# Kernel optimization log

Measured on AMD Instinct MI355X. Metric: run time of the kernel, lower is better.

Reference implementation:

```python
import jax, jax.numpy as jnp
import numpy as np

QBITS = 8
QMIN, QMAX = -(2 ** (QBITS - 1)), 2 ** (QBITS - 1) - 1  # qint8: -128..127


def fq_act(x):
    """Per-tensor affine fake-quant (observer = min/max of tensor), with STE."""
    mn = jnp.minimum(jnp.min(x), 0.0)
    mx = jnp.maximum(jnp.max(x), 0.0)
    scale = jnp.maximum((mx - mn) / (QMAX - QMIN), 1e-8)
    zp = QMIN - jnp.round(mn / scale)
    q = jnp.clip(jnp.round(x / scale) + zp, QMIN, QMAX)
    y = (q - zp) * scale
    return x + jax.lax.stop_gradient(y - x)


def fq_w(w):
    """Per-tensor symmetric weight fake-quant, with STE."""
    scale = jnp.maximum(jnp.max(jnp.abs(w)) / QMAX, 1e-8)
    y = jnp.clip(jnp.round(w / scale), QMIN, QMAX) * scale
    return w + jax.lax.stop_gradient(y - w)


def setup_inputs() -> dict:
    key = jax.random.key(0)
    ks = jax.random.split(key, 8)
    B, T, F, K = 32, 1024, 512, 31
    return {
        "x": jax.random.normal(ks[0], (B, T, F), jnp.float32),
        "ln_scale": jnp.ones((F,), jnp.float32),
        "ln_bias": jnp.zeros((F,), jnp.float32),
        "w1": jax.random.normal(ks[1], (2 * F, F), jnp.float32) * 0.02,
        "b1": jax.random.normal(ks[2], (2 * F,), jnp.float32) * 0.02,
        "dw_w": jax.random.normal(ks[3], (F, 1, K), jnp.float32) * 0.1,
        "dw_b": jax.random.normal(ks[4], (F,), jnp.float32) * 0.02,
        "bn_gamma": jnp.ones((F,), jnp.float32),
        "bn_beta": jnp.zeros((F,), jnp.float32),
        "bn_mean": jnp.zeros((F,), jnp.float32),
        "bn_var": jax.random.uniform(ks[5], (F,), jnp.float32, 0.5, 1.5),
        "w2": jax.random.normal(ks[6], (F, F), jnp.float32) * 0.02,
        "b2": jax.random.normal(ks[7], (F,), jnp.float32) * 0.02,
    }


def reference(x, ln_scale, ln_bias, w1, b1, dw_w, dw_b,
              bn_gamma, bn_beta, bn_mean, bn_var, w2, b2):
    F = x.shape[-1]
    # --- custom L1 layer norm, fake-quant in/out ---
    t = fq_act(x)
    t = t - jnp.mean(t, axis=-1, keepdims=True)
    t = t / (jnp.sum(jnp.abs(t), axis=-1, keepdims=True) / F + 1e-5)
    t = t * ln_scale + ln_bias
    t = fq_act(t)
    # --- pointwise conv 1 (linear F -> 2F), quant-wrapped ---
    t = fq_act(t)
    t = jnp.einsum("btf,of->bto", t, fq_w(w1)) + b1
    t = fq_act(t)
    # --- GLU, quant-wrapped ---
    t = fq_act(t)
    a, g = jnp.split(t, 2, axis=-1)
    t = a * jax.nn.sigmoid(g)
    t = fq_act(t)
    # --- depthwise conv over time, quant-wrapped ---
    t = jnp.transpose(t, (0, 2, 1))  # [B,F,T]
    t = fq_act(t)
    t = jax.lax.conv_general_dilated(
        t, fq_w(dw_w), window_strides=(1,), padding=[((dw_w.shape[-1] - 1) // 2,) * 2],
        dimension_numbers=("NCH", "OIH", "NCH"), feature_group_count=F,
    ) + dw_b[:, None]
    t = fq_act(t)
    # --- batch norm (eval mode, running stats), quant-wrapped ---
    t = fq_act(t)
    t = (t - bn_mean[:, None]) * (bn_gamma[:, None] / jnp.sqrt(bn_var[:, None] + 1e-5)) + bn_beta[:, None]
    t = fq_act(t)
    t = jnp.transpose(t, (0, 2, 1))  # [B,T,F]
    # --- SiLU activation, quant-wrapped ---
    t = fq_act(t)
    t = jax.nn.silu(t)
    t = fq_act(t)
    # --- pointwise conv 2 (linear F -> F), quant-wrapped ---
    t = fq_act(t)
    t = jnp.einsum("btf,of->bto", t, fq_w(w2)) + b2
    t = fq_act(t)
    return t  # dropout is identity at eval
```

## Files before the change

kernel.cpp:

```cpp
#include <hip/hip_runtime.h>
#include <stdint.h>
#include <math.h>

#define INF __builtin_inff()

typedef __attribute__((ext_vector_type(4))) float f32x4;
typedef __attribute__((ext_vector_type(8))) short s16x8;
typedef __attribute__((ext_vector_type(4))) short s16x4;
typedef __attribute__((ext_vector_type(4))) char c8x4;

#define S_XMN 0
#define S_XMX 1
#define S_T1MN 2
#define S_T1MX 3
#define S_T4MN 4
#define S_T4MX 5
#define S_T7MN 6
#define S_T7MX 7
#define S_CVMN 8
#define S_CVMX 9
#define S_BNMN 10
#define S_BNMX 11
#define S_SIMN 12
#define S_SIMX 13
#define S_T18MN 14
#define S_T18MX 15
#define S_W1 16
#define S_W2 17
#define S_DW 18
#define NSLOT 19

#define NTOT 16777216L

__device__ __forceinline__ unsigned enc(float f) {
  unsigned u = __float_as_uint(f);
  return (u & 0x80000000u) ? ~u : (u | 0x80000000u);
}
__device__ __forceinline__ float dec(unsigned k) {
  return (k & 0x80000000u) ? __uint_as_float(k & 0x7FFFFFFFu) : __uint_as_float(~k);
}

struct FQ { float s, zp; };

__device__ __forceinline__ FQ fq_params(float mn_t, float mx_t) {
  float mn = fminf(mn_t, 0.0f), mx = fmaxf(mx_t, 0.0f);
  FQ p;
  p.s = fmaxf((mx - mn) / 255.0f, 1e-8f);
  p.zp = -128.0f - rintf(mn / p.s);
  return p;
}
__device__ __forceinline__ float fq_apply(float x, FQ p) {
  float q = rintf(x / p.s) + p.zp;
  q = fminf(fmaxf(q, -128.0f), 127.0f);
  return (q - p.zp) * p.s;
}
__device__ __forceinline__ float fq_qmz(float x, FQ p) {
  float q = rintf(x / p.s) + p.zp;
  q = fminf(fmaxf(q, -128.0f), 127.0f);
  return q - p.zp;
}
__device__ __forceinline__ int qidx(float x, FQ p) {
  float q = rintf(x / p.s) + p.zp;
  q = fminf(fmaxf(q, -128.0f), 127.0f);
  return (int)q + 128;
}
__device__ __forceinline__ int qcode(float x, FQ p) {
  float q = rintf(x / p.s) + p.zp;
  q = fminf(fmaxf(q, -128.0f), 127.0f);
  return (int)q;
}
__device__ __forceinline__ void fq_pair(const unsigned* slots, int idx, FQ& p1, FQ& p2) {
  float mn = dec(slots[idx]), mx = dec(slots[idx + 1]);
  p1 = fq_params(mn, mx);
  float ymn = fq_apply(mn, p1), ymx = fq_apply(mx, p1);
  p2 = fq_params(ymn, ymx);
}
__device__ __forceinline__ unsigned short to_bf16(float v) {
  return (unsigned short)(__float_as_uint(v) >> 16);
}

__device__ __forceinline__ void mm_block_atomic(float mn, float mx, unsigned* smn, unsigned* smx) {
#pragma unroll
  for (int o = 32; o > 0; o >>= 1) {
    mn = fminf(mn, __shfl_down(mn, o, 64));
    mx = fmaxf(mx, __shfl_down(mx, o, 64));
  }
  __shared__ float rmn[16], rmx[16];
  int lane = threadIdx.x & 63, wid = threadIdx.x >> 6;
  int nw = blockDim.x >> 6;
  __syncthreads();
  if (lane == 0) { rmn[wid] = mn; rmx[wid] = mx; }
  __syncthreads();
  if (threadIdx.x == 0) {
    for (int i = 1; i < nw; ++i) { mn = fminf(mn, rmn[i]); mx = fmaxf(mx, rmx[i]); }
    atomicMin(smn, enc(mn));
    atomicMax(smx, enc(mx));
  }
}

__device__ __forceinline__ float wave_sum(float v) {
#pragma unroll
  for (int o = 1; o < 64; o <<= 1) v += __shfl_xor(v, o, 64);
  return v;
}

__global__ void k_init(unsigned* __restrict__ slots, const float* __restrict__ gm,
                       const float* __restrict__ vr, float* __restrict__ gs) {
  int i = threadIdx.x;
  if (i < NSLOT) slots[i] = (i < 16) ? ((i & 1) ? enc(-INF) : enc(INF)) : enc(0.0f);
  gs[i] = gm[i] / sqrtf(vr[i] + 1e-5f);
}

__global__ __launch_bounds__(256) void k_redmm(const float* __restrict__ x, unsigned* __restrict__ slots) {
  long i = ((long)blockIdx.x * 256 + threadIdx.x) * 4;
  const long stride = (long)2048 * 256 * 4;
  float mn = INF, mx = -INF;
  for (; i < NTOT; i += stride) {
    f32x4 v = *(const f32x4*)(x + i);
    mn = fminf(mn, fminf(fminf(v.x, v.y), fminf(v.z, v.w)));
    mx = fmaxf(mx, fmaxf(fmaxf(v.x, v.y), fmaxf(v.z, v.w)));
  }
  mm_block_atomic(mn, mx, slots + S_XMN, slots + S_XMX);
}

__global__ __launch_bounds__(256) void k_wabs(const float* __restrict__ w1, const float* __restrict__ w2,
                                              const float* __restrict__ dw, unsigned* __restrict__ slots) {
  int b = blockIdx.x;
  const float* p; int slot; long base;
  if (b < 2048) { p = w1; slot = S_W1; base = (long)b * 256; }
  else if (b < 3072) { p = w2; slot = S_W2; base = (long)(b - 2048) * 256; }
  else { p = dw; slot = S_DW; base = (long)(b - 3072) * 256; }
  float v = fabsf(p[base + threadIdx.x]);
#pragma unroll
  for (int o = 32; o > 0; o >>= 1) v = fmaxf(v, __shfl_down(v, o, 64));
  __shared__ float r[4];
  int lane = threadIdx.x & 63, wid = threadIdx.x >> 6;
  if (lane == 0) r[wid] = v;
  __syncthreads();
  if (threadIdx.x == 0) {
    v = fmaxf(fmaxf(r[0], r[1]), fmaxf(r[2], r[3]));
    atomicMax(slots + slot, enc(v));
  }
}

__global__ __launch_bounds__(256) void k_wq(const float* __restrict__ w1, const float* __restrict__ w2,
    const float* __restrict__ dw, unsigned short* __restrict__ w1q, unsigned short* __restrict__ w2q,
    float* __restrict__ dwq, const unsigned* __restrict__ slots) {
  int b = blockIdx.x;
  if (b < 2048) {
    float s = fmaxf(dec(slots[S_W1]) / 127.0f, 1e-8f);
    long i = (long)b * 256 + threadIdx.x;
    float q = fminf(fmaxf(rintf(w1[i] / s), -128.0f), 127.0f);
    w1q[i] = to_bf16(q);
  } else if (b < 3072) {
    float s = fmaxf(dec(slots[S_W2]) / 127.0f, 1e-8f);
    long i = (long)(b - 2048) * 256 + threadIdx.x;
    float q = fminf(fmaxf(rintf(w2[i] / s), -128.0f), 127.0f);
    w2q[i] = to_bf16(q);
  } else {
    float s = fmaxf(dec(slots[S_DW]) / 127.0f, 1e-8f);
    long i = (long)(b - 3072) * 256 + threadIdx.x;
    float q = fminf(fmaxf(rintf(dw[i] / s), -128.0f), 127.0f);
    dwq[i] = q;
  }
}

__device__ __forceinline__ void ln_core(float* a, const f32x4& sc0, const f32x4& sc1,
                                        const f32x4& bi0, const f32x4& bi1) {
  float s = a[0] + a[1] + a[2] + a[3] + a[4] + a[5] + a[6] + a[7];
  float mean = wave_sum(s) / 512.0f;
#pragma unroll
  for (int j = 0; j < 8; ++j) a[j] -= mean;
  float l1 = fabsf(a[0]) + fabsf(a[1]) + fabsf(a[2]) + fabsf(a[3])
           + fabsf(a[4]) + fabsf(a[5]) + fabsf(a[6]) + fabsf(a[7]);
  float denom = wave_sum(l1) / 512.0f + 1e-5f;
#pragma unroll
  for (int j = 0; j < 4; ++j) {
    a[j]     = fmaf(a[j] / denom,     sc0[j], bi0[j]);
    a[4 + j] = fmaf(a[4 + j] / denom, sc1[j], bi1[j]);
  }
}

__global__ __launch_bounds__(256) void k_lnmm(const float* __restrict__ x, const float* __restrict__ lns,
    const float* __restrict__ lnb, signed char* __restrict__ qx, unsigned* __restrict__ slots) {
  FQ p0 = fq_params(dec(slots[S_XMN]), dec(slots[S_XMX]));
  int lane = threadIdx.x & 63, wv = threadIdx.x >> 6;
  long gw = (long)blockIdx.x * 4 + wv;
  f32x4 sc0 = *(const f32x4*)(lns + lane * 4);
  f32x4 sc1 = *(const f32x4*)(lns + 256 + lane * 4);
  f32x4 bi0 = *(const f32x4*)(lnb + lane * 4);
  f32x4 bi1 = *(const f32x4*)(lnb + 256 + lane * 4);
  float lmn = INF, lmx = -INF;
  for (int r = 0; r < 4; ++r) {
    long row = gw + (long)r * 8192;
    f32x4 v0 = *(const f32x4*)(x + row * 512 + lane * 4);
    f32x4 v1 = *(const f32x4*)(x + row * 512 + 256 + lane * 4);
    float a[8];
    c8x4 c0, c1;
#pragma unroll
    for (int j = 0; j < 4; ++j) {
      int q0 = qcode(v0[j], p0), q1 = qcode(v1[j], p0);
      c0[j] = (signed char)q0; c1[j] = (signed char)q1;
      a[j]     = ((float)q0 - p0.zp) * p0.s;
      a[4 + j] = ((float)q1 - p0.zp) * p0.s;
    }
    *(c8x4*)(qx + row * 512 + lane * 4) = c0;
    *(c8x4*)(qx + row * 512 + 256 + lane * 4) = c1;
    ln_core(a, sc0, sc1, bi0, bi1);
#pragma unroll
    for (int j = 0; j < 8; ++j) { lmn = fminf(lmn, a[j]); lmx = fmaxf(lmx, a[j]); }
  }
  mm_block_atomic(lmn, lmx, slots + S_T1MN, slots + S_T1MX);
}

__global__ __launch_bounds__(256) void k_qa(const signed char* __restrict__ qx, const float* __restrict__ lns,
    const float* __restrict__ lnb, unsigned short* __restrict__ A1, const unsigned* __restrict__ slots) {
  __shared__ unsigned short lut[256];
  FQ p0 = fq_params(dec(slots[S_XMN]), dec(slots[S_XMX]));
  FQ p1, p2; fq_pair(slots, S_T1MN, p1, p2);
  {
    int i = threadIdx.x;
    float y1 = ((float)(i - 128) - p1.zp) * p1.s;
    lut[i] = to_bf16(fq_qmz(y1, p2));
  }
  __syncthreads();
  int lane = threadIdx.x & 63, wv = threadIdx.x >> 6;
  long gw = (long)blockIdx.x * 4 + wv;
  f32x4 sc0 = *(const f32x4*)(lns + lane * 4);
  f32x4 sc1 = *(const f32x4*)(lns + 256 + lane * 4);
  f32x4 bi0 = *(const f32x4*)(lnb + lane * 4);
  f32x4 bi1 = *(const f32x4*)(lnb + 256 + lane * 4);
  for (int r = 0; r < 4; ++r) {
    long row = gw + (long)r * 8192;
    c8x4 c0 = *(const c8x4*)(qx + row * 512 + lane * 4);
    c8x4 c1 = *(const c8x4*)(qx + row * 512 + 256 + lane * 4);
    float a[8];
#pragma unroll
    for (int j = 0; j < 4; ++j) {
      a[j]     = ((float)(int)c0[j] - p0.zp) * p0.s;
      a[4 + j] = ((float)(int)c1[j] - p0.zp) * p0.s;
    }
    ln_core(a, sc0, sc1, bi0, bi1);
    s16x4 q0, q1;
#pragma unroll
    for (int j = 0; j < 4; ++j) {
      q0[j] = (short)lut[qidx(a[j], p1)];
      q1[j] = (short)lut[qidx(a[4 + j], p1)];
    }
    *(s16x4*)(A1 + row * 512 + lane * 4) = q0;
    *(s16x4*)(A1 + row * 512 + 256 + lane * 4) = q1;
  }
}

__global__ __launch_bounds__(256) void k_gemm(const unsigned short* __restrict__ A,
    const unsigned short* __restrict__ Bm, const float* __restrict__ bias,
    float* __restrict__ C, int N, unsigned* __restrict__ slots, int mmIdx, int wIdx, int omIdx) {
  __shared__ __align__(16) unsigned short lA[128 * 64];
  __shared__ __align__(16) unsigned short lB[128 * 64];
  FQ p1, p2; fq_pair(slots, mmIdx, p1, p2);
  float sw = fmaxf(dec(slots[wIdx]) / 127.0f, 1e-8f);
  float sAB = p2.s * sw;
  int tid = threadIdx.x;
  int nbx = gridDim.x;
  int total = nbx * gridDim.y;
  int id = blockIdx.y * nbx + blockIdx.x;
  int chunk = total >> 3;
  int d = (id & 7) * chunk + (id >> 3);
  int m0 = (d / nbx) * 128, n0 = (d % nbx) * 128;
  int lane = tid & 63, wid = tid >> 6;
  int wm = (wid >> 1) * 64, wn = (wid & 1) * 64;
  const f32x4 fz = {0.0f, 0.0f, 0.0f, 0.0f};
  f32x4 acc[4][4];
#pragma unroll
  for (int mi = 0; mi < 4; ++mi)
#pragma unroll
    for (int ni = 0; ni < 4; ++ni) acc[mi][ni] = fz;
  int sr = tid >> 1;
  int scu = (tid & 1) * 32;
  int swz = (sr & 7) * 8;
  const unsigned short* Ag = A + (long)(m0 + sr) * 512 + scu;
  const unsigned short* Bg = Bm + (long)(n0 + sr) * 512 + scu;
  int fr = lane & 15;
  int fc = (lane >> 4) * 8;
  for (int kt = 0; kt < 8; ++kt) {
    s16x8 ra[4], rb[4];
#pragma unroll
    for (int j = 0; j < 4; ++j) {
      ra[j] = *(const s16x8*)(Ag + kt * 64 + j * 8);
      rb[j] = *(const s16x8*)(Bg + kt * 64 + j * 8);
    }
    __syncthreads();
#pragma unroll
    for (int j = 0; j < 4; ++j) {
      *(s16x8*)&lA[sr * 64 + ((scu + j * 8) ^ swz)] = ra[j];
      *(s16x8*)&lB[sr * 64 + ((scu + j * 8) ^ swz)] = rb[j];
    }
    __syncthreads();
#pragma unroll
    for (int ks = 0; ks < 2; ++ks) {
      s16x8 af[4], bfv[4];
#pragma unroll
      for (int mi = 0; mi < 4; ++mi) {
        int r = wm + mi * 16 + fr;
        af[mi] = *(const s16x8*)&lA[r * 64 + ((ks * 32 + fc) ^ ((r & 7) * 8))];
      }
#pragma unroll
      for (int ni = 0; ni < 4; ++ni) {
        int r = wn + ni * 16 + fr;
        bfv[ni] = *(const s16x8*)&lB[r * 64 + ((ks * 32 + fc) ^ ((r & 7) * 8))];
      }
#pragma unroll
      for (int mi = 0; mi < 4; ++mi)
#pragma unroll
        for (int ni = 0; ni < 4; ++ni)
          acc[mi][ni] = __builtin_amdgcn_mfma_f32_16x16x32_bf16(af[mi], bfv[ni], acc[mi][ni], 0, 0, 0);
    }
  }
  float lmn = INF, lmx = -INF;
  int rb0 = m0 + wm + ((lane >> 4) << 2);
  int cb0 = n0 + wn + (lane & 15);
#pragma unroll
  for (int mi = 0; mi < 4; ++mi) {
#pragma unroll
    for (int ni = 0; ni < 4; ++ni) {
      int col = cb0 + ni * 16;
      float bv = bias[col];
#pragma unroll
      for (int r = 0; r < 4; ++r) {
        int rowi = rb0 + mi * 16 + r;
        float v = sAB * acc[mi][ni][r] + bv;
        C[(long)rowi * N + col] = v;
        lmn = fminf(lmn, v); lmx = fmaxf(lmx, v);
      }
    }
  }
  mm_block_atomic(lmn, lmx, slots + omIdx, slots + omIdx + 1);
}

__global__ __launch_bounds__(256) void k_glu(const float* __restrict__ t4, unsigned short* __restrict__ pair,
                                             unsigned* __restrict__ slots) {
  __shared__ float lutf[256];
  __shared__ float sglut[256];
  FQ p1, p2; fq_pair(slots, S_T4MN, p1, p2);
  {
    int i = threadIdx.x;
    float y2 = fq_apply(((float)(i - 128) - p1.zp) * p1.s, p2);
    lutf[i] = y2;
    sglut[i] = 1.0f / (1.0f + expf(-y2));
  }
  __syncthreads();
  long i = ((long)blockIdx.x * 256 + threadIdx.x) * 4;
  const long stride = (long)2048 * 256 * 4;
  float lmn = INF, lmx = -INF;
  for (; i < NTOT; i += stride) {
    long r = i >> 9;
    int c = (int)(i & 511);
    const float* pa = t4 + r * 1024 + c;
    f32x4 av = *(const f32x4*)pa;
    f32x4 gv = *(const f32x4*)(pa + 512);
    s16x4 o;
#pragma unroll
    for (int j = 0; j < 4; ++j) {
      int qa = qidx(av[j], p1);
      int qg = qidx(gv[j], p1);
      o[j] = (short)(unsigned short)(qa | (qg << 8));
      float y = lutf[qa] * sglut[qg];
      lmn = fminf(lmn, y); lmx = fmaxf(lmx, y);
    }
    *(s16x4*)(pair + i) = o;
  }
  mm_block_atomic(lmn, lmx, slots + S_T7MN, slots + S_T7MX);
}

__global__ __launch_bounds__(256) void k_qt7(const unsigned short* __restrict__ pair,
                                             signed char* __restrict__ q7,
                                             const unsigned* __restrict__ slots) {
  __shared__ float lutf[256];
  __shared__ float sglut[256];
  __shared__ signed char lutq[256];
  FQ g1, g2; fq_pair(slots, S_T4MN, g1, g2);
  FQ p1, p2; fq_pair(slots, S_T7MN, p1, p2);
  {
    int i = threadIdx.x;
    float y2 = fq_apply(((float)(i - 128) - g1.zp) * g1.s, g2);
    lutf[i] = y2;
    sglut[i] = 1.0f / (1.0f + expf(-y2));
    float y1 = ((float)(i - 128) - p1.zp) * p1.s;
    float q = fminf(fmaxf(rintf(y1 / p2.s) + p2.zp, -128.0f), 127.0f);
    lutq[i] = (signed char)(int)q;
  }
  __syncthreads();
  long i = ((long)blockIdx.x * 256 + threadIdx.x) * 4;
  const long stride = (long)2048 * 256 * 4;
  for (; i < NTOT; i += stride) {
    s16x4 pv = *(const s16x4*)(pair + i);
    c8x4 o;
#pragma unroll
    for (int j = 0; j < 4; ++j) {
      unsigned u = (unsigned short)pv[j];
      float y = lutf[u & 255] * sglut[u >> 8];
      o[j] = lutq[qidx(y, p1)];
    }
    *(c8x4*)(q7 + i) = o;
  }
}

template<int STORE>
__global__ __launch_bounds__(256) void k_conv(const signed char* __restrict__ q7,
    const float* __restrict__ dwq, const float* __restrict__ dwb,
    signed char* __restrict__ qcv, const float* __restrict__ gs, const float* __restrict__ mu,
    const float* __restrict__ bt, unsigned* __restrict__ slots) {
  __shared__ signed char lutq[256];
  FQ p1, p2; fq_pair(slots, S_T7MN, p1, p2);
  float sdw = fmaxf(dec(slots[S_DW]) / 127.0f, 1e-8f);
  float scv = p2.s * sdw;
  float zp2 = p2.zp;
  FQ c1, c2;
  if (STORE) {
    fq_pair(slots, S_CVMN, c1, c2);
    int i = threadIdx.x;
    float y1 = ((float)(i - 128) - c1.zp) * c1.s;
    float q = fminf(fmaxf(rintf(y1 / c2.s) + c2.zp, -128.0f), 127.0f);
    lutq[i] = (signed char)(int)q;
    __syncthreads();
  }
  int t0 = blockIdx.x * 32;
  int f = blockIdx.y * 256 + threadIdx.x;
  int b = blockIdx.z;
  const signed char* base = q7 + (long)b * 1024 * 512 + f;
  float col[62];
#pragma unroll
  for (int r = 0; r < 62; ++r) {
    int t = t0 - 15 + r;
    float q = 0.0f;
    if ((unsigned)t < 1024u) q = (float)(int)base[(long)t * 512] - zp2;
    col[r] = q;
  }
  float w31[31];
#pragma unroll
  for (int k = 0; k < 31; ++k) w31[k] = dwq[f * 31 + k];
  float bias = dwb[f];
  float gsv = 0.f, muv = 0.f, btv = 0.f;
  if (STORE) { gsv = gs[f]; muv = mu[f]; btv = bt[f]; }
  signed char* orow = STORE ? (qcv + ((long)b * 1024 + t0) * 512 + f) : nullptr;
  float lmn = INF, lmx = -INF;
#pragma unroll
  for (int j = 0; j < 32; ++j) {
    float acc = 0.0f;
#pragma unroll
    for (int k = 0; k < 31; ++k) acc += col[j + k] * w31[k];
    float v = fmaf(scv, acc, bias);
    if (STORE) {
      signed char qc = lutq[qidx(v, c1)];
      orow[(long)j * 512] = qc;
      float y2 = ((float)(int)qc - c2.zp) * c2.s;
      float z = fmaf(y2 - muv, gsv, btv);
      lmn = fminf(lmn, z); lmx = fmaxf(lmx, z);
    } else {
      lmn = fminf(lmn, v); lmx = fmaxf(lmx, v);
    }
  }
  if (STORE) mm_block_atomic(lmn, lmx, slots + S_BNMN, slots + S_BNMX);
  else       mm_block_atomic(lmn, lmx, slots + S_CVMN, slots + S_CVMX);
}

__global__ __launch_bounds__(256) void k_silumm(const signed char* __restrict__ qcv,
    const float* __restrict__ gs, const float* __restrict__ mu, const float* __restrict__ bt,
    unsigned* __restrict__ slots) {
  __shared__ float sillut[256];
  FQ c1, c2; fq_pair(slots, S_CVMN, c1, c2);
  FQ b1q, b2q; fq_pair(slots, S_BNMN, b1q, b2q);
  {
    int i = threadIdx.x;
    float z2 = fq_apply(((float)(i - 128) - b1q.zp) * b1q.s, b2q);
    sillut[i] = z2 * (1.0f / (1.0f + expf(-z2)));
  }
  __syncthreads();
  float s2 = c2.s, zp2 = c2.zp;
  long i = ((long)blockIdx.x * 256 + threadIdx.x) * 4;
  const long stride = (long)2048 * 256 * 4;
  float lmn = INF, lmx = -INF;
  for (; i < NTOT; i += stride) {
    int f0 = (int)(i & 511);
    c8x4 qv = *(const c8x4*)(qcv + i);
    f32x4 g4 = *(const f32x4*)(gs + f0);
    f32x4 m4 = *(const f32x4*)(mu + f0);
    f32x4 b4 = *(const f32x4*)(bt + f0);
#pragma unroll
    for (int j = 0; j < 4; ++j) {
      float y2 = ((float)(int)qv[j] - zp2) * s2;
      float z = fmaf(y2 - m4[j], g4[j], b4[j]);
      float si = sillut[qidx(z, b1q)];
      lmn = fminf(lmn, si); lmx = fmaxf(lmx, si);
    }
  }
  mm_block_atomic(lmn, lmx, slots + S_SIMN, slots + S_SIMX);
}

__global__ __launch_bounds__(256) void k_q2(const signed char* __restrict__ qcv,
    const float* __restrict__ gs, const float* __restrict__ mu, const float* __restrict__ bt,
    unsigned short* __restrict__ A2, const unsigned* __restrict__ slots) {
  __shared__ unsigned short lutc[256];
  FQ c1, c2; fq_pair(slots, S_CVMN, c1, c2);
  FQ b1q, b2q; fq_pair(slots, S_BNMN, b1q, b2q);
  FQ s1q, s2q; fq_pair(slots, S_SIMN, s1q, s2q);
  {
    int i = threadIdx.x;
    float z2 = fq_apply(((float)(i - 128) - b1q.zp) * b1q.s, b2q);
    float si = z2 * (1.0f / (1.0f + expf(-z2)));
    float ys = ((float)(qidx(si, s1q) - 128) - s1q.zp) * s1q.s;
    lutc[i] = to_bf16(fq_qmz(ys, s2q));
  }
  __syncthreads();
  float s2 = c2.s, zp2 = c2.zp;
  long i = ((long)blockIdx.x * 256 + threadIdx.x) * 4;
  const long stride = (long)2048 * 256 * 4;
  for (; i < NTOT; i += stride) {
    int f0 = (int)(i & 511);
    c8x4 qv = *(const c8x4*)(qcv + i);
    f32x4 g4 = *(const f32x4*)(gs + f0);
    f32x4 m4 = *(const f32x4*)(mu + f0);
    f32x4 b4 = *(const f32x4*)(bt + f0);
    s16x4 o;
#pragma unroll
    for (int j = 0; j < 4; ++j) {
      float y2 = ((float)(int)qv[j] - zp2) * s2;
      float z = fmaf(y2 - m4[j], g4[j], b4[j]);
      o[j] = (short)lutc[qidx(z, b1q)];
    }
    *(s16x4*)(A2 + i) = o;
  }
}

__global__ __launch_bounds__(256) void k_final(const float* __restrict__ t18, float* __restrict__ out,
                                               const unsigned* __restrict__ slots) {
  FQ p = fq_params(dec(slots[S_T18MN]), dec(slots[S_T18MX]));
  long i = ((long)blockIdx.x * 256 + threadIdx.x) * 4;
  const long stride = (long)2048 * 256 * 4;
  for (; i < NTOT; i += stride) {
    f32x4 v = *(const f32x4*)(t18 + i);
    f32x4 o;
#pragma unroll
    for (int j = 0; j < 4; ++j) o[j] = fq_apply(v[j], p);
    *(f32x4*)(out + i) = o;
  }
}

extern "C" void kernel_launch(void* const* d_in, const int* in_sizes, int n_in,
                              void* d_out, int out_size, void* d_ws, size_t ws_size,
                              hipStream_t stream) {
  const float* x   = (const float*)d_in[0];
  const float* lns = (const float*)d_in[1];
  const float* lnb = (const float*)d_in[2];
  const float* w1  = (const float*)d_in[3];
  const float* b1  = (const float*)d_in[4];
  const float* dw  = (const float*)d_in[5];
  const float* dwb = (const float*)d_in[6];
  const float* gm  = (const float*)d_in[7];
  const float* bt  = (const float*)d_in[8];
  const float* mu  = (const float*)d_in[9];
  const float* vr  = (const float*)d_in[10];
  const float* w2  = (const float*)d_in[11];
  const float* b2  = (const float*)d_in[12];
  float* out = (float*)d_out;
  char* ws = (char*)d_ws;

  const size_t O_A2  = 16777216;
  const size_t O_T18 = 50331648;
  const size_t O_A1  = 134217728;
  const size_t O_QX  = 167772160;
  const size_t O_WQ  = 184549376;
  const size_t NEED = O_WQ + 1048576 + 524288 + 63488 + 2048 + 256;
  if (ws_size < NEED) return;

  float* t4   = (float*)ws;
  signed char* qcv = (signed char*)ws;
  unsigned short* A2 = (unsigned short*)(ws + O_A2);
  float* t18  = (float*)(ws + O_T18);
  unsigned short* A1 = (unsigned short*)(ws + O_A1);
  unsigned short* pair = (unsigned short*)(ws + O_A1);
  signed char* qx = (signed char*)(ws + O_QX);
  signed char* q7 = (signed char*)(ws + O_QX);
  unsigned short* w1q = (unsigned short*)(ws + O_WQ);
  unsigned short* w2q = (unsigned short*)(ws + O_WQ + 1048576);
  float* dwq = (float*)(ws + O_WQ + 1048576 + 524288);
  float* gs  = (float*)(ws + O_WQ + 1048576 + 524288 + 63488);
  unsigned* slots = (unsigned*)(ws + O_WQ + 1048576 + 524288 + 63488 + 2048);

  k_init<<<1, 512, 0, stream>>>(slots, gm, vr, gs);
  k_wabs<<<3134, 256, 0, stream>>>(w1, w2, dw, slots);
  k_wq<<<3134, 256, 0, stream>>>(w1, w2, dw, w1q, w2q, dwq, slots);
  k_redmm<<<2048, 256, 0, stream>>>(x, slots);
  k_lnmm<<<2048, 256, 0, stream>>>(x, lns, lnb, qx, slots);
  k_qa<<<2048, 256, 0, stream>>>(qx, lns, lnb, A1, slots);
  k_gemm<<<dim3(8, 256), 256, 0, stream>>>(A1, w1q, b1, t4, 1024, slots, S_T1MN, S_W1, S_T4MN);
  k_glu<<<2048, 256, 0, stream>>>(t4, pair, slots);
  k_qt7<<<2048, 256, 0, stream>>>(pair, q7, slots);
  k_conv<0><<<dim3(32, 2, 32), 256, 0, stream>>>(q7, dwq, dwb, nullptr, gs, mu, bt, slots);
  k_conv<1><<<dim3(32, 2, 32), 256, 0, stream>>>(q7, dwq, dwb, qcv, gs, mu, bt, slots);
  k_silumm<<<2048, 256, 0, stream>>>(qcv, gs, mu, bt, slots);
  k_q2<<<2048, 256, 0, stream>>>(qcv, gs, mu, bt, A2, slots);
  k_gemm<<<dim3(4, 256), 256, 0, stream>>>(A2, w2q, b2, t18, 512, slots, S_SIMN, S_W2, S_T18MN);
  k_final<<<2048, 256, 0, stream>>>(t18, out, slots);
}
```

Measured before the change: 731.6 us.

## Use direct global-to-LDS loads in GEMM and transpose depthwise weights

The GEMM tile loads now use global_load_lds to write 16-byte chunks straight into LDS, replacing the register staging pass. The source addresses are XOR-swizzled so the existing read swizzle still matches, and the first-iteration barrier is skipped. Depthwise conv weights are stored transposed as [k][f] so each thread's weight loads coalesce across f. The conv inner product is split into four independent accumulators with launch_bounds(256,1), which shortens the FMA dependency chain at the cost of register pressure and a changed float summation order.

```diff
diff --git a/kernel.cpp b/kernel.cpp
--- a/kernel.cpp
+++ b/kernel.cpp
@@ -79,6 +79,12 @@
   return (unsigned short)(__float_as_uint(v) >> 16);
 }
 
+__device__ __forceinline__ void gload_lds16(const void* g, void* l) {
+  __builtin_amdgcn_global_load_lds(
+      (const __attribute__((address_space(1))) unsigned int*)g,
+      (__attribute__((address_space(3))) unsigned int*)l, 16, 0, 0);
+}
+
 __device__ __forceinline__ void mm_block_atomic(float mn, float mx, unsigned* smn, unsigned* smx) {
 #pragma unroll
   for (int o = 32; o > 0; o >>= 1) {
@@ -145,7 +151,7 @@
 
 __global__ __launch_bounds__(256) void k_wq(const float* __restrict__ w1, const float* __restrict__ w2,
     const float* __restrict__ dw, unsigned short* __restrict__ w1q, unsigned short* __restrict__ w2q,
-    float* __restrict__ dwq, const unsigned* __restrict__ slots) {
+    float* __restrict__ dwqT, const unsigned* __restrict__ slots) {
   int b = blockIdx.x;
   if (b < 2048) {
     float s = fmaxf(dec(slots[S_W1]) / 127.0f, 1e-8f);
@@ -159,9 +165,10 @@
     w2q[i] = to_bf16(q);
   } else {
     float s = fmaxf(dec(slots[S_DW]) / 127.0f, 1e-8f);
-    long i = (long)(b - 3072) * 256 + threadIdx.x;
+    int i = (b - 3072) * 256 + threadIdx.x;
+    int f = i / 31, k = i % 31;
     float q = fminf(fmaxf(rintf(dw[i] / s), -128.0f), 127.0f);
-    dwq[i] = q;
+    dwqT[k * 512 + f] = q;
   }
 }
 
@@ -267,33 +274,35 @@
   int chunk = total >> 3;
   int d = (id & 7) * chunk + (id >> 3);
   int m0 = (d / nbx) * 128, n0 = (d % nbx) * 128;
-  int lane = tid & 63, wid = tid >> 6;
-  int wm = (wid >> 1) * 64, wn = (wid & 1) * 64;
+  int lane = tid & 63, w = tid >> 6;
+  int wm = (w >> 1) * 64, wn = (w & 1) * 64;
   const f32x4 fz = {0.0f, 0.0f, 0.0f, 0.0f};
   f32x4 acc[4][4];
 #pragma unroll
   for (int mi = 0; mi < 4; ++mi)
 #pragma unroll
     for (int ni = 0; ni < 4; ++ni) acc[mi][ni] = fz;
-  int sr = tid >> 1;
-  int scu = (tid & 1) * 32;
-  int swz = (sr & 7) * 8;
-  const unsigned short* Ag = A + (long)(m0 + sr) * 512 + scu;
-  const unsigned short* Bg = Bm + (long)(n0 + sr) * 512 + scu;
+  int r8 = lane >> 3;
+  int c8 = (lane & 7) * 8;
+  int srcc = c8 ^ (r8 * 8);
+  const unsigned short* Abase[4];
+  const unsigned short* Bbase[4];
+#pragma unroll
+  for (int i = 0; i < 4; ++i) {
+    int row = w * 32 + i * 8 + r8;
+    Abase[i] = A + (long)(m0 + row) * 512 + srcc;
+    Bbase[i] = Bm + (long)(n0 + row) * 512 + srcc;
+  }
+  char* lAc = (char*)lA;
+  char* lBc = (char*)lB;
   int fr = lane & 15;
   int fc = (lane >> 4) * 8;
   for (int kt = 0; kt < 8; ++kt) {
-    s16x8 ra[4], rb[4];
-#pragma unroll
-    for (int j = 0; j < 4; ++j) {
-      ra[j] = *(const s16x8*)(Ag + kt * 64 + j * 8);
-      rb[j] = *(const s16x8*)(Bg + kt * 64 + j * 8);
-    }
-    __syncthreads();
-#pragma unroll
-    for (int j = 0; j < 4; ++j) {
-      *(s16x8*)&lA[sr * 64 + ((scu + j * 8) ^ swz)] = ra[j];
-      *(s16x8*)&lB[sr * 64 + ((scu + j * 8) ^ swz)] = rb[j];
+    if (kt) __syncthreads();
+#pragma unroll
+    for (int i = 0; i < 4; ++i) {
+      gload_lds16(Abase[i] + kt * 64, lAc + (w * 4 + i) * 1024);
+      gload_lds16(Bbase[i] + kt * 64, lBc + (w * 4 + i) * 1024);
     }
     __syncthreads();
 #pragma unroll
@@ -406,8 +415,8 @@
 }
 
 template<int STORE>
-__global__ __launch_bounds__(256) void k_conv(const signed char* __restrict__ q7,
-    const float* __restrict__ dwq, const float* __restrict__ dwb,
+__global__ __launch_bounds__(256, 1) void k_conv(const signed char* __restrict__ q7,
+    const float* __restrict__ dwqT, const float* __restrict__ dwb,
     signed char* __restrict__ qcv, const float* __restrict__ gs, const float* __restrict__ mu,
     const float* __restrict__ bt, unsigned* __restrict__ slots) {
   __shared__ signed char lutq[256];
@@ -436,9 +445,9 @@
     if ((unsigned)t < 1024u) q = (float)(int)base[(long)t * 512] - zp2;
     col[r] = q;
   }
-  float w31[31];
-#pragma unroll
-  for (int k = 0; k < 31; ++k) w31[k] = dwq[f * 31 + k];
+  float wv[31];
+#pragma unroll
+  for (int k = 0; k < 31; ++k) wv[k] = dwqT[k * 512 + f];
   float bias = dwb[f];
   float gsv = 0.f, muv = 0.f, btv = 0.f;
   if (STORE) { gsv = gs[f]; muv = mu[f]; btv = bt[f]; }
@@ -446,9 +455,18 @@
   float lmn = INF, lmx = -INF;
 #pragma unroll
   for (int j = 0; j < 32; ++j) {
-    float acc = 0.0f;
-#pragma unroll
-    for (int k = 0; k < 31; ++k) acc += col[j + k] * w31[k];
+    float a0 = 0.f, a1 = 0.f, a2 = 0.f, a3 = 0.f;
+#pragma unroll
+    for (int k = 0; k < 28; k += 4) {
+      a0 += col[j + k]     * wv[k];
+      a1 += col[j + k + 1] * wv[k + 1];
+      a2 += col[j + k + 2] * wv[k + 2];
+      a3 += col[j + k + 3] * wv[k + 3];
+    }
+    a0 += col[j + 28] * wv[28];
+    a1 += col[j + 29] * wv[29];
+    a2 += col[j + 30] * wv[30];
+    float acc = (a0 + a1) + (a2 + a3);
     float v = fmaf(scv, acc, bias);
     if (STORE) {
       signed char qc = lutq[qidx(v, c1)];
@@ -583,21 +601,21 @@
   signed char* q7 = (signed char*)(ws + O_QX);
   unsigned short* w1q = (unsigned short*)(ws + O_WQ);
   unsigned short* w2q = (unsigned short*)(ws + O_WQ + 1048576);
-  float* dwq = (float*)(ws + O_WQ + 1048576 + 524288);
+  float* dwqT = (float*)(ws + O_WQ + 1048576 + 524288);
   float* gs  = (float*)(ws + O_WQ + 1048576 + 524288 + 63488);
   unsigned* slots = (unsigned*)(ws + O_WQ + 1048576 + 524288 + 63488 + 2048);
 
   k_init<<<1, 512, 0, stream>>>(slots, gm, vr, gs);
   k_wabs<<<3134, 256, 0, stream>>>(w1, w2, dw, slots);
-  k_wq<<<3134, 256, 0, stream>>>(w1, w2, dw, w1q, w2q, dwq, slots);
+  k_wq<<<3134, 256, 0, stream>>>(w1, w2, dw, w1q, w2q, dwqT, slots);
   k_redmm<<<2048, 256, 0, stream>>>(x, slots);
   k_lnmm<<<2048, 256, 0, stream>>>(x, lns, lnb, qx, slots);
   k_qa<<<2048, 256, 0, stream>>>(qx, lns, lnb, A1, slots);
   k_gemm<<<dim3(8, 256), 256, 0, stream>>>(A1, w1q, b1, t4, 1024, slots, S_T1MN, S_W1, S_T4MN);
   k_glu<<<2048, 256, 0, stream>>>(t4, pair, slots);
   k_qt7<<<2048, 256, 0, stream>>>(pair, q7, slots);
-  k_conv<0><<<dim3(32, 2, 32), 256, 0, stream>>>(q7, dwq, dwb, nullptr, gs, mu, bt, slots);
-  k_conv<1><<<dim3(32, 2, 32), 256, 0, stream>>>(q7, dwq, dwb, qcv, gs, mu, bt, slots);
+  k_conv<0><<<dim3(32, 2, 32), 256, 0, stream>>>(q7, dwqT, dwb, nullptr, gs, mu, bt, slots);
+  k_conv<1><<<dim3(32, 2, 32), 256, 0, stream>>>(q7, dwqT, dwb, qcv, gs, mu, bt, slots);
   k_silumm<<<2048, 256, 0, stream>>>(qcv, gs, mu, bt, slots);
   k_q2<<<2048, 256, 0, stream>>>(qcv, gs, mu, bt, A2, slots);
   k_gemm<<<dim3(4, 256), 256, 0, stream>>>(A2, w2q, b2, t18, 512, slots, S_SIMN, S_W2, S_T18MN);
```

Measured after the change: 719.7 us. Within noise of the previous version (-1.6%).
